# Performance work log

Hardware: AMD Instinct MI355X
Metric: run time of the kernel (lower is better)

## Reference

```python
import jax, jax.numpy as jnp
import numpy as np

N = 50000
E = 400000
NEG_SLOPE = 0.2


def gat_conv(x, src, dst, W, a_src, a_dst, b, heads, out_ch):
    """PyG-style GATConv with self-loops already included in (src, dst).
    src/dst: [E2] edge endpoints; messages flow src -> dst; softmax over in-edges per dst.
    """
    n = x.shape[0]
    h = (x @ W).reshape(n, heads, out_ch)               # [N, H, C]
    es = jnp.sum(h * a_src, axis=-1)                    # [N, H] alpha_src per node
    ed = jnp.sum(h * a_dst, axis=-1)                    # [N, H] alpha_dst per node
    e = jax.nn.leaky_relu(es[src] + ed[dst], NEG_SLOPE)  # [E2, H] raw scores
    # segment softmax over destination neighborhoods (stable)
    m = jax.ops.segment_max(e, dst, num_segments=n)     # [N, H]
    p = jnp.exp(e - m[dst])
    s = jax.ops.segment_sum(p, dst, num_segments=n)     # [N, H]
    alpha = p / s[dst]                                  # [E2, H]
    agg = jax.ops.segment_sum(h[src] * alpha[..., None], dst, num_segments=n)  # [N, H, C]
    return agg.reshape(n, heads * out_ch) + b


def setup_inputs() -> dict:
    key = jax.random.key(0)
    ks = jax.random.split(key, 14)
    rn = lambda k, shape, s=0.1: (jax.random.normal(k, shape, dtype=jnp.float32) * s)
    x = jax.random.normal(ks[0], (N, 21), dtype=jnp.float32)
    edge_index = jax.random.randint(ks[1], (2, E), 0, N, dtype=jnp.int32)
    return {
        "x": x,
        "W1": rn(ks[2], (21, 4 * 128)), "a_src1": rn(ks[3], (4, 128)), "a_dst1": rn(ks[4], (4, 128)), "b1": rn(ks[5], (512,)),
        "W2": rn(ks[6], (512, 64)), "a_src2": rn(ks[7], (1, 64)), "a_dst2": rn(ks[8], (1, 64)), "b2": rn(ks[9], (64,)),
        "W3": rn(ks[10], (64, 1)), "a_src3": rn(ks[11], (1, 1)), "a_dst3": rn(ks[12], (1, 1)), "b3": rn(ks[13], (1,)),
        "edge_index": edge_index,
    }


def reference(x, W1, a_src1, a_dst1, b1, W2, a_src2, a_dst2, b2, W3, a_src3, a_dst3, b3, edge_index):
    loops = jnp.arange(N, dtype=edge_index.dtype)
    src = jnp.concatenate([edge_index[0], loops])  # add self loops (PyG default)
    dst = jnp.concatenate([edge_index[1], loops])
    h1 = jax.nn.elu(gat_conv(x, src, dst, W1, a_src1, a_dst1, b1, heads=4, out_ch=128))   # [N, 512]
    h2 = jax.nn.elu(gat_conv(h1, src, dst, W2, a_src2, a_dst2, b2, heads=1, out_ch=64))   # [N, 64]
    h3 = gat_conv(h2, src, dst, W3, a_src3, a_dst3, b3, heads=1, out_ch=1)                # [N, 1]
    return h3.mean(axis=0)  # [1]
```

## Files before the change

### kernel.cpp

```cpp
#include <hip/hip_runtime.h>
#include <hip/hip_fp16.h>
#include <math.h>

#define N_NODES 50000
#define E_EDGES 400000
#define NEG_SLOPE 0.2f
#define SCAN_BLOCKS 250
#define SCAN_CHUNK 200

typedef _Float16 f16x8 __attribute__((ext_vector_type(8)));
typedef float f32x4 __attribute__((ext_vector_type(4)));

static inline int cdiv(long a, int b) { return (int)((a + b - 1) / b); }

__device__ __forceinline__ float lrelu(float v) {
    return v > 0.f ? v : NEG_SLOPE * v;
}

__device__ __forceinline__ void h4_to_f4(uint2 u, float o[4]) {
    union { uint2 u2; __half h[4]; } cv;
    cv.u2 = u;
    #pragma unroll
    for (int i = 0; i < 4; ++i) o[i] = __half2float(cv.h[i]);
}

__global__ void k_count(const int* __restrict__ ei, int* __restrict__ deg) {
    int e = blockIdx.x * blockDim.x + threadIdx.x;
    if (e >= E_EDGES) return;
    atomicAdd(&deg[ei[E_EDGES + e]], 1);
}

__global__ void k_scan1(const int* __restrict__ deg, int* __restrict__ bsum) {
    __shared__ int sd[256];
    int b = blockIdx.x, t = threadIdx.x;
    int lo = b * SCAN_CHUNK;
    int s = 0;
    for (int i = t; i < SCAN_CHUNK; i += 256) s += deg[lo + i];
    sd[t] = s;
    __syncthreads();
    for (int off = 128; off; off >>= 1) {
        if (t < off) sd[t] += sd[t + off];
        __syncthreads();
    }
    if (t == 0) bsum[b] = sd[0];
}

__global__ void k_scan2(int* __restrict__ bsum) {
    __shared__ int sd[256];
    int t = threadIdx.x;
    int v = (t < SCAN_BLOCKS) ? bsum[t] : 0;
    sd[t] = v;
    __syncthreads();
    for (int off = 1; off < 256; off <<= 1) {
        int u = (t >= off) ? sd[t - off] : 0;
        __syncthreads();
        sd[t] += u;
        __syncthreads();
    }
    if (t < SCAN_BLOCKS) bsum[t] = sd[t] - v;
}

__global__ void k_scan3(const int* __restrict__ deg, const int* __restrict__ bsum,
                        int* __restrict__ row_ptr) {
    __shared__ int sd[256];
    int b = blockIdx.x, t = threadIdx.x;
    int lo = b * SCAN_CHUNK;
    int v = (t < SCAN_CHUNK) ? deg[lo + t] : 0;
    sd[t] = v;
    __syncthreads();
    for (int off = 1; off < 256; off <<= 1) {
        int u = (t >= off) ? sd[t - off] : 0;
        __syncthreads();
        sd[t] += u;
        __syncthreads();
    }
    if (t < SCAN_CHUNK) row_ptr[lo + t] = bsum[b] + sd[t] - v;
    if (b == 0 && t == 0) row_ptr[N_NODES] = E_EDGES;
}

__global__ void k_scatter(const int* __restrict__ ei, const int* __restrict__ row_ptr,
                          int* __restrict__ pos, int* __restrict__ csr_src) {
    int e = blockIdx.x * blockDim.x + threadIdx.x;
    if (e >= E_EDGES) return;
    int src = ei[e], dst = ei[E_EDGES + e];
    int p = atomicAdd(&pos[dst], 1);
    csr_src[row_ptr[dst] + p] = src;
}

__global__ void k_l1_coef(const float* __restrict__ x, const float* __restrict__ W1,
                          const float* __restrict__ a_src, const float* __restrict__ a_dst,
                          float* __restrict__ es, float* __restrict__ ed) {
    __shared__ float wesS[88], wedS[88];
    const int t = threadIdx.x;
    if (t < 168) {
        int which = t / 84;
        int idx = t % 84;
        int k = idx >> 2, h = idx & 3;
        const float* a = which ? a_dst : a_src;
        float s = 0.f;
        for (int c = 0; c < 128; ++c)
            s += W1[k * 512 + h * 128 + c] * a[h * 128 + c];
        (which ? wedS : wesS)[idx] = s;
    }
    __syncthreads();

    int node = blockIdx.x * blockDim.x + t;
    if (node >= N_NODES) return;
    const float* xr = x + (size_t)node * 21;
    float e1[4] = {0.f, 0.f, 0.f, 0.f}, e2[4] = {0.f, 0.f, 0.f, 0.f};
    #pragma unroll
    for (int k = 0; k < 21; ++k) {
        float xv = xr[k];
        float4 a = *(const float4*)&wesS[k * 4];
        float4 b = *(const float4*)&wedS[k * 4];
        e1[0] += xv * a.x; e1[1] += xv * a.y; e1[2] += xv * a.z; e1[3] += xv * a.w;
        e2[0] += xv * b.x; e2[1] += xv * b.y; e2[2] += xv * b.z; e2[3] += xv * b.w;
    }
    *(float4*)&es[node * 4] = make_float4(e1[0], e1[1], e1[2], e1[3]);
    *(float4*)&ed[node * 4] = make_float4(e2[0], e2[1], e2[2], e2[3]);
}

__global__ void k_edge_l1x(const int* __restrict__ row_ptr, const int* __restrict__ csr_src,
                           const float* __restrict__ x, const float* __restrict__ es,
                           const float* __restrict__ ed, __half* __restrict__ y16) {
    int wid = (blockIdx.x * blockDim.x + threadIdx.x) >> 6;
    int l = threadIdx.x & 63;
    if (wid >= N_NODES) return;
    const int dst = wid;
    const int hh = l >> 4, sub = l & 15;
    const int beg = row_ptr[dst], end = row_ptr[dst + 1];
    const float eddg = ed[dst * 4 + hh];
    const float self_v = lrelu(es[dst * 4 + hh] + eddg);

    float s = 0.f;
    for (int k = beg + sub; k < end; k += 16)
        s += __expf(lrelu(es[csr_src[k] * 4 + hh] + eddg));
    #pragma unroll
    for (int off = 1; off < 16; off <<= 1) s += __shfl_xor(s, off, 64);
    float p_self = __expf(self_v);
    s += p_self;
    float inv_s = 1.f / s;

    float ih[4], eh[4], ph[4];
    #pragma unroll
    for (int h = 0; h < 4; ++h) {
        ih[h] = __shfl(inv_s, h * 16, 64);
        eh[h] = __shfl(eddg, h * 16, 64);
        ph[h] = __shfl(p_self, h * 16, 64);
    }

    const int g = l / 21;
    const int c = l - g * 21;
    const bool act = (l < 63);

    float xdv = (act && g == 0) ? x[(size_t)dst * 21 + c] : 0.f;
    float acc[4];
    #pragma unroll
    for (int h = 0; h < 4; ++h) acc[h] = ph[h] * ih[h] * xdv;

    if (act) {
        int k = beg + g;
        for (; k + 3 < end; k += 6) {
            int s0 = csr_src[k], s1 = csr_src[k + 3];
            float4 e0 = *(const float4*)&es[s0 * 4];
            float4 e1 = *(const float4*)&es[s1 * 4];
            float x0 = x[(size_t)s0 * 21 + c];
            float x1 = x[(size_t)s1 * 21 + c];
            #pragma unroll
            for (int h = 0; h < 4; ++h) {
                float a0 = __expf(lrelu((&e0.x)[h] + eh[h])) * ih[h];
                float a1 = __expf(lrelu((&e1.x)[h] + eh[h])) * ih[h];
                acc[h] += a0 * x0 + a1 * x1;
            }
        }
        if (k < end) {
            int s0 = csr_src[k];
            float4 e0 = *(const float4*)&es[s0 * 4];
            float x0 = x[(size_t)s0 * 21 + c];
            #pragma unroll
            for (int h = 0; h < 4; ++h) {
                float a0 = __expf(lrelu((&e0.x)[h] + eh[h])) * ih[h];
                acc[h] += a0 * x0;
            }
        }
    }

    #pragma unroll
    for (int h = 0; h < 4; ++h) {
        float a1 = __shfl(acc[h], (l + 21) & 63, 64);
        float a2 = __shfl(acc[h], (l + 42) & 63, 64);
        acc[h] += a1 + a2;
    }
    if (l < 32) {
        #pragma unroll
        for (int h = 0; h < 4; ++h) {
            float v = (l < 21) ? acc[h] : 0.f;
            y16[(size_t)dst * 128 + h * 32 + l] = __float2half_rn(v);
        }
    }
}

__global__ void k_wt(const float* __restrict__ W1, const float* __restrict__ W2,
                     __half* __restrict__ W1t, __half* __restrict__ W2t) {
    int idx = blockIdx.x * blockDim.x + threadIdx.x;
    if (idx < 512 * 32) {
        int n = idx >> 5, k = idx & 31;
        W1t[idx] = (k < 21) ? __float2half_rn(W1[k * 512 + n]) : __half(0.f);
    } else {
        int j = idx - 512 * 32;
        if (j < 512 * 64) {
            int k = j >> 6, n = j & 63;
            W2t[(size_t)n * 512 + k] = __float2half_rn(W2[j]);
        }
    }
}

__global__ void k_l12_fused(const __half* __restrict__ y16, const __half* __restrict__ W1t,
                            const float* __restrict__ b1, const __half* __restrict__ W2t,
                            const float* __restrict__ a_src, const float* __restrict__ a_dst,
                            __half* __restrict__ C16, float* __restrict__ es, float* __restrict__ ed) {
    __shared__ _Float16 As[32][520];
    __shared__ float p1s[32][4];
    __shared__ float p2s[32][4];

    const int t = threadIdx.x;
    const int l = t & 63;
    const int wv = t >> 6;
    const int row0 = blockIdx.x * 32;
    const int lr = l & 15;
    const int kg = l >> 4;

    const _Float16* Y = (const _Float16*)y16;
    const _Float16* B1 = (const _Float16*)W1t;

    int ra0 = row0 + lr;       ra0 = ra0 < N_NODES ? ra0 : N_NODES - 1;
    int ra1 = row0 + 16 + lr;  ra1 = ra1 < N_NODES ? ra1 : N_NODES - 1;

    f32x4 acc1[2][8];
    #pragma unroll
    for (int m = 0; m < 2; ++m)
        #pragma unroll
        for (int n = 0; n < 8; ++n) acc1[m][n] = (f32x4){0.f, 0.f, 0.f, 0.f};

    f16x8 a0 = *(const f16x8*)(Y + (size_t)ra0 * 128 + wv * 32 + kg * 8);
    f16x8 a1 = *(const f16x8*)(Y + (size_t)ra1 * 128 + wv * 32 + kg * 8);

    #pragma unroll
    for (int nt = 0; nt < 8; ++nt) {
        f16x8 bf = *(const f16x8*)(B1 + (size_t)(wv * 128 + nt * 16 + lr) * 32 + kg * 8);
        acc1[0][nt] = __builtin_amdgcn_mfma_f32_16x16x32_f16(a0, bf, acc1[0][nt], 0, 0, 0);
        acc1[1][nt] = __builtin_amdgcn_mfma_f32_16x16x32_f16(a1, bf, acc1[1][nt], 0, 0, 0);
    }

    float bb[8];
    #pragma unroll
    for (int nt = 0; nt < 8; ++nt) bb[nt] = b1[wv * 128 + nt * 16 + lr];

    #pragma unroll
    for (int m = 0; m < 2; ++m) {
        #pragma unroll
        for (int r = 0; r < 4; ++r) {
            int rl = m * 16 + kg * 4 + r;
            #pragma unroll
            for (int nt = 0; nt < 8; ++nt) {
                float v = acc1[m][nt][r] + bb[nt];
                v = v > 0.f ? v : __expf(v) - 1.f;
                As[rl][wv * 128 + nt * 16 + lr] = (_Float16)v;
            }
        }
    }
    __syncthreads();

    const _Float16* B2 = (const _Float16*)W2t;
    const int n_g = wv * 16 + lr;
    f32x4 acc2[2];
    acc2[0] = (f32x4){0.f, 0.f, 0.f, 0.f};
    acc2[1] = (f32x4){0.f, 0.f, 0.f, 0.f};

    for (int kb = 0; kb < 512; kb += 32) {
        f16x8 fa0 = *(const f16x8*)&As[lr][kb + kg * 8];
        f16x8 fa1 = *(const f16x8*)&As[16 + lr][kb + kg * 8];
        f16x8 bf = *(const f16x8*)(B2 + (size_t)n_g * 512 + kb + kg * 8);
        acc2[0] = __builtin_amdgcn_mfma_f32_16x16x32_f16(fa0, bf, acc2[0], 0, 0, 0);
        acc2[1] = __builtin_amdgcn_mfma_f32_16x16x32_f16(fa1, bf, acc2[1], 0, 0, 0);
    }

    const float asv = a_src[n_g];
    const float adv = a_dst[n_g];

    #pragma unroll
    for (int m = 0; m < 2; ++m) {
        #pragma unroll
        for (int r = 0; r < 4; ++r) {
            int rl = m * 16 + kg * 4 + r;
            int grow = row0 + rl;
            float cv = acc2[m][r];
            float p1 = cv * asv, p2 = cv * adv;
            #pragma unroll
            for (int off = 1; off < 16; off <<= 1) {
                p1 += __shfl_xor(p1, off, 64);
                p2 += __shfl_xor(p2, off, 64);
            }
            if (grow < N_NODES)
                C16[(size_t)grow * 64 + n_g] = __float2half_rn(cv);
            if (lr == 0) { p1s[rl][wv] = p1; p2s[rl][wv] = p2; }
        }
    }
    __syncthreads();

    if (t < 32) {
        int grow = row0 + t;
        if (grow < N_NODES) {
            es[grow] = p1s[t][0] + p1s[t][1] + p1s[t][2] + p1s[t][3];
            ed[grow] = p2s[t][0] + p2s[t][1] + p2s[t][2] + p2s[t][3];
        }
    }
}

__global__ void k_gat_edge_l2_l3(const int* __restrict__ row_ptr, const int* __restrict__ csr_src,
                                 const __half* __restrict__ h16, const float* __restrict__ es,
                                 const float* __restrict__ ed, const float* __restrict__ b,
                                 const float* __restrict__ W3, const float* __restrict__ a_src3,
                                 const float* __restrict__ a_dst3, float* __restrict__ h3,
                                 float* __restrict__ es3, float* __restrict__ ed3) {
    int wid = (blockIdx.x * blockDim.x + threadIdx.x) >> 6;
    int lane = threadIdx.x & 63;
    if (wid >= N_NODES) return;
    const int dst = wid;
    const int g = lane >> 4, sub = lane & 15;
    const int beg = row_ptr[dst], end = row_ptr[dst + 1];
    const float edd = ed[dst];
    const float self_v = lrelu(es[dst] + edd);

    float s = 0.f;
    for (int k = beg + lane; k < end; k += 64)
        s += __expf(lrelu(es[csr_src[k]] + edd));
    #pragma unroll
    for (int off = 32; off; off >>= 1) s += __shfl_xor(s, off, 64);
    float p_self = __expf(self_v);
    s += p_self;
    const float inv_s = 1.f / s;

    float acc[4] = {0.f, 0.f, 0.f, 0.f};
    if (g == 0) {
        uint2 r = *(const uint2*)(h16 + (size_t)dst * 64 + sub * 4);
        float hv[4]; h4_to_f4(r, hv);
        float a_self = p_self * inv_s;
        #pragma unroll
        for (int j = 0; j < 4; ++j) acc[j] = a_self * hv[j];
    }
    for (int k0 = beg; k0 < end; k0 += 4) {
        int k = k0 + g;
        if (k < end) {
            int src = csr_src[k];
            float alpha = __expf(lrelu(es[src] + edd)) * inv_s;
            uint2 r = *(const uint2*)(h16 + (size_t)src * 64 + sub * 4);
            float hv[4]; h4_to_f4(r, hv);
            #pragma unroll
            for (int j = 0; j < 4; ++j) acc[j] += alpha * hv[j];
        }
    }
    #pragma unroll
    for (int off = 16; off < 64; off <<= 1) {
        #pragma unroll
        for (int j = 0; j < 4; ++j) acc[j] += __shfl_xor(acc[j], off, 64);
    }

    float4 bv = *(const float4*)&b[sub * 4];
    float4 w3 = *(const float4*)&W3[sub * 4];
    float o0 = acc[0] + bv.x, o1 = acc[1] + bv.y, o2 = acc[2] + bv.z, o3 = acc[3] + bv.w;
    o0 = o0 > 0.f ? o0 : expm1f(o0);
    o1 = o1 > 0.f ? o1 : expm1f(o1);
    o2 = o2 > 0.f ? o2 : expm1f(o2);
    o3 = o3 > 0.f ? o3 : expm1f(o3);
    float pp = o0 * w3.x + o1 * w3.y + o2 * w3.z + o3 * w3.w;
    #pragma unroll
    for (int off = 1; off < 16; off <<= 1) pp += __shfl_xor(pp, off, 64);

    if (lane == 0) {
        h3[dst] = pp;
        es3[dst] = pp * a_src3[0];
        ed3[dst] = pp * a_dst3[0];
    }
}

__global__ void k_gat_edge_c1_mean(const int* __restrict__ row_ptr, const int* __restrict__ csr_src,
                                   const float* __restrict__ h, const float* __restrict__ es,
                                   const float* __restrict__ ed, const float* __restrict__ b3,
                                   float* __restrict__ out) {
    __shared__ float sdata[256];
    int dst = blockIdx.x * blockDim.x + threadIdx.x;
    float val = 0.f;
    if (dst < N_NODES) {
        int beg = row_ptr[dst], end = row_ptr[dst + 1];
        float edd = ed[dst];
        float self_v = lrelu(es[dst] + edd);
        float p = __expf(self_v);
        float s = p;
        float acc = p * h[dst];
        for (int k = beg; k < end; ++k) {
            int src = csr_src[k];
            float pv = __expf(lrelu(es[src] + edd));
            s += pv;
            acc += pv * h[src];
        }
        val = acc / s;
    }
    sdata[threadIdx.x] = val;
    __syncthreads();
    for (int sft = 128; sft > 0; sft >>= 1) {
        if (threadIdx.x < sft) sdata[threadIdx.x] += sdata[threadIdx.x + sft];
        __syncthreads();
    }
    if (threadIdx.x == 0) {
        float add = sdata[0] / (float)N_NODES;
        if (blockIdx.x == 0) add += b3[0];
        atomicAdd(out, add);
    }
}

extern "C" void kernel_launch(void* const* d_in, const int* in_sizes, int n_in,
                              void* d_out, int out_size, void* d_ws, size_t ws_size,
                              hipStream_t stream) {
    const float* x      = (const float*)d_in[0];
    const float* W1     = (const float*)d_in[1];
    const float* a_src1 = (const float*)d_in[2];
    const float* a_dst1 = (const float*)d_in[3];
    const float* b1     = (const float*)d_in[4];
    const float* W2     = (const float*)d_in[5];
    const float* a_src2 = (const float*)d_in[6];
    const float* a_dst2 = (const float*)d_in[7];
    const float* b2     = (const float*)d_in[8];
    const float* W3     = (const float*)d_in[9];
    const float* a_src3 = (const float*)d_in[10];
    const float* a_dst3 = (const float*)d_in[11];
    const float* b3     = (const float*)d_in[12];
    const int*   ei     = (const int*)d_in[13];
    float* out = (float*)d_out;

    const int BS = 256;
    const size_t N = N_NODES;

    float*  ws      = (float*)d_ws;
    __half* y16     = (__half*)ws;
    __half* h2_16   = (__half*)(ws + N * 64);
    float*  h3raw   = ws + N * 96;
    float*  es3     = h3raw + N;
    float*  ed3     = es3 + N;
    float*  es_buf  = ed3 + N;
    float*  ed_buf  = es_buf + N * 4;
    __half* W1t     = (__half*)(ed_buf + N * 4);
    __half* W2t     = (__half*)(ed_buf + N * 4 + 8192);
    int*    deg     = (int*)(ed_buf + N * 4 + 8192 + 16384);
    int*    row_ptr = deg + N;
    int*    csr_src = row_ptr + N + 1;
    int*    bsum    = csr_src + E_EDGES;

    hipMemsetAsync(deg, 0, N * sizeof(int), stream);
    k_count<<<cdiv(E_EDGES, BS), BS, 0, stream>>>(ei, deg);
    k_scan1<<<SCAN_BLOCKS, 256, 0, stream>>>(deg, bsum);
    k_scan2<<<1, 256, 0, stream>>>(bsum);
    k_scan3<<<SCAN_BLOCKS, 256, 0, stream>>>(deg, bsum, row_ptr);
    hipMemsetAsync(deg, 0, N * sizeof(int), stream);
    k_scatter<<<cdiv(E_EDGES, BS), BS, 0, stream>>>(ei, row_ptr, deg, csr_src);

    k_l1_coef<<<cdiv((long)N, BS), BS, 0, stream>>>(x, W1, a_src1, a_dst1, es_buf, ed_buf);
    k_edge_l1x<<<cdiv((long)N * 64, BS), BS, 0, stream>>>(row_ptr, csr_src, x, es_buf, ed_buf, y16);

    k_wt<<<cdiv(512 * 32 + 512 * 64, BS), BS, 0, stream>>>(W1, W2, W1t, W2t);
    k_l12_fused<<<cdiv(N_NODES, 32), 256, 0, stream>>>(y16, W1t, b1, W2t, a_src2, a_dst2, h2_16, es_buf, ed_buf);

    k_gat_edge_l2_l3<<<cdiv((long)N * 64, BS), BS, 0, stream>>>(row_ptr, csr_src, h2_16, es_buf, ed_buf,
                                                                b2, W3, a_src3, a_dst3, h3raw, es3, ed3);

    hipMemsetAsync(out, 0, sizeof(float), stream);
    k_gat_edge_c1_mean<<<cdiv((long)N, BS), BS, 0, stream>>>(row_ptr, csr_src, h3raw, es3, ed3, b3, out);
}
```

Before: 165.9 us.

## Fuse prep kernels, drop scatter memset, parallelize final layer edge loop

Merges degree counting, the weight transposes and the layer-1 coefficient computation into one prep kernel, removing two launches. The CSR scatter now increments row_ptr itself, so row_ptr ends up holding segment ends and consumers read begin from row_ptr[dst-1]; this drops the second memset and the separate position array. The final mean kernel now uses 16 lanes per destination with shuffle reductions instead of one thread per node. Trade-offs are a different CSR ordering within rows (already nondeterministic) and a __syncthreads inside a block-conditional branch in the prep kernel.

```diff
diff --git a/kernel.cpp b/kernel.cpp
--- a/kernel.cpp
+++ b/kernel.cpp
@@ -24,10 +24,56 @@
     for (int i = 0; i < 4; ++i) o[i] = __half2float(cv.h[i]);
 }
 
-__global__ void k_count(const int* __restrict__ ei, int* __restrict__ deg) {
-    int e = blockIdx.x * blockDim.x + threadIdx.x;
-    if (e >= E_EDGES) return;
-    atomicAdd(&deg[ei[E_EDGES + e]], 1);
+__global__ void k_prep(const int* __restrict__ ei, int* __restrict__ deg,
+                       const float* __restrict__ x, const float* __restrict__ W1,
+                       const float* __restrict__ a_src, const float* __restrict__ a_dst,
+                       float* __restrict__ es, float* __restrict__ ed,
+                       const float* __restrict__ W2, __half* __restrict__ W1t,
+                       __half* __restrict__ W2t) {
+    __shared__ float wesS[88], wedS[88];
+    const int t = threadIdx.x;
+    const int gid = blockIdx.x * blockDim.x + t;
+
+    if (gid < E_EDGES) atomicAdd(&deg[ei[E_EDGES + gid]], 1);
+
+    if (gid < 512 * 32) {
+        int n = gid >> 5, k = gid & 31;
+        W1t[gid] = (k < 21) ? __float2half_rn(W1[k * 512 + n]) : __half(0.f);
+    } else if (gid < 512 * 32 + 512 * 64) {
+        int j = gid - 512 * 32;
+        int k = j >> 6, n = j & 63;
+        W2t[(size_t)n * 512 + k] = __float2half_rn(W2[j]);
+    }
+
+    if (blockIdx.x < (N_NODES + 255) / 256) {
+        if (t < 168) {
+            int which = t / 84;
+            int idx = t % 84;
+            int k = idx >> 2, h = idx & 3;
+            const float* a = which ? a_dst : a_src;
+            float s = 0.f;
+            for (int c = 0; c < 128; ++c)
+                s += W1[k * 512 + h * 128 + c] * a[h * 128 + c];
+            (which ? wedS : wesS)[idx] = s;
+        }
+        __syncthreads();
+
+        int node = blockIdx.x * blockDim.x + t;
+        if (node < N_NODES) {
+            const float* xr = x + (size_t)node * 21;
+            float e1[4] = {0.f, 0.f, 0.f, 0.f}, e2[4] = {0.f, 0.f, 0.f, 0.f};
+            #pragma unroll
+            for (int k = 0; k < 21; ++k) {
+                float xv = xr[k];
+                float4 a = *(const float4*)&wesS[k * 4];
+                float4 b = *(const float4*)&wedS[k * 4];
+                e1[0] += xv * a.x; e1[1] += xv * a.y; e1[2] += xv * a.z; e1[3] += xv * a.w;
+                e2[0] += xv * b.x; e2[1] += xv * b.y; e2[2] += xv * b.z; e2[3] += xv * b.w;
+            }
+            *(float4*)&es[node * 4] = make_float4(e1[0], e1[1], e1[2], e1[3]);
+            *(float4*)&ed[node * 4] = make_float4(e2[0], e2[1], e2[2], e2[3]);
+        }
+    }
 }
 
 __global__ void k_scan1(const int* __restrict__ deg, int* __restrict__ bsum) {
@@ -75,49 +121,15 @@
         __syncthreads();
     }
     if (t < SCAN_CHUNK) row_ptr[lo + t] = bsum[b] + sd[t] - v;
-    if (b == 0 && t == 0) row_ptr[N_NODES] = E_EDGES;
-}
-
-__global__ void k_scatter(const int* __restrict__ ei, const int* __restrict__ row_ptr,
-                          int* __restrict__ pos, int* __restrict__ csr_src) {
+}
+
+__global__ void k_scatter(const int* __restrict__ ei, int* __restrict__ row_ptr,
+                          int* __restrict__ csr_src) {
     int e = blockIdx.x * blockDim.x + threadIdx.x;
     if (e >= E_EDGES) return;
     int src = ei[e], dst = ei[E_EDGES + e];
-    int p = atomicAdd(&pos[dst], 1);
-    csr_src[row_ptr[dst] + p] = src;
-}
-
-__global__ void k_l1_coef(const float* __restrict__ x, const float* __restrict__ W1,
-                          const float* __restrict__ a_src, const float* __restrict__ a_dst,
-                          float* __restrict__ es, float* __restrict__ ed) {
-    __shared__ float wesS[88], wedS[88];
-    const int t = threadIdx.x;
-    if (t < 168) {
-        int which = t / 84;
-        int idx = t % 84;
-        int k = idx >> 2, h = idx & 3;
-        const float* a = which ? a_dst : a_src;
-        float s = 0.f;
-        for (int c = 0; c < 128; ++c)
-            s += W1[k * 512 + h * 128 + c] * a[h * 128 + c];
-        (which ? wedS : wesS)[idx] = s;
-    }
-    __syncthreads();
-
-    int node = blockIdx.x * blockDim.x + t;
-    if (node >= N_NODES) return;
-    const float* xr = x + (size_t)node * 21;
-    float e1[4] = {0.f, 0.f, 0.f, 0.f}, e2[4] = {0.f, 0.f, 0.f, 0.f};
-    #pragma unroll
-    for (int k = 0; k < 21; ++k) {
-        float xv = xr[k];
-        float4 a = *(const float4*)&wesS[k * 4];
-        float4 b = *(const float4*)&wedS[k * 4];
-        e1[0] += xv * a.x; e1[1] += xv * a.y; e1[2] += xv * a.z; e1[3] += xv * a.w;
-        e2[0] += xv * b.x; e2[1] += xv * b.y; e2[2] += xv * b.z; e2[3] += xv * b.w;
-    }
-    *(float4*)&es[node * 4] = make_float4(e1[0], e1[1], e1[2], e1[3]);
-    *(float4*)&ed[node * 4] = make_float4(e2[0], e2[1], e2[2], e2[3]);
+    int p = atomicAdd(&row_ptr[dst], 1);
+    csr_src[p] = src;
 }
 
 __global__ void k_edge_l1x(const int* __restrict__ row_ptr, const int* __restrict__ csr_src,
@@ -128,7 +140,8 @@
     if (wid >= N_NODES) return;
     const int dst = wid;
     const int hh = l >> 4, sub = l & 15;
-    const int beg = row_ptr[dst], end = row_ptr[dst + 1];
+    const int beg = dst ? row_ptr[dst - 1] : 0;
+    const int end = row_ptr[dst];
     const float eddg = ed[dst * 4 + hh];
     const float self_v = lrelu(es[dst * 4 + hh] + eddg);
 
@@ -196,21 +209,6 @@
         for (int h = 0; h < 4; ++h) {
             float v = (l < 21) ? acc[h] : 0.f;
             y16[(size_t)dst * 128 + h * 32 + l] = __float2half_rn(v);
-        }
-    }
-}
-
-__global__ void k_wt(const float* __restrict__ W1, const float* __restrict__ W2,
-                     __half* __restrict__ W1t, __half* __restrict__ W2t) {
-    int idx = blockIdx.x * blockDim.x + threadIdx.x;
-    if (idx < 512 * 32) {
-        int n = idx >> 5, k = idx & 31;
-        W1t[idx] = (k < 21) ? __float2half_rn(W1[k * 512 + n]) : __half(0.f);
-    } else {
-        int j = idx - 512 * 32;
-        if (j < 512 * 64) {
-            int k = j >> 6, n = j & 63;
-            W2t[(size_t)n * 512 + k] = __float2half_rn(W2[j]);
         }
     }
 }
@@ -328,7 +326,8 @@
     if (wid >= N_NODES) return;
     const int dst = wid;
     const int g = lane >> 4, sub = lane & 15;
-    const int beg = row_ptr[dst], end = row_ptr[dst + 1];
+    const int beg = dst ? row_ptr[dst - 1] : 0;
+    const int end = row_ptr[dst];
     const float edd = ed[dst];
     const float self_v = lrelu(es[dst] + edd);
 
@@ -389,30 +388,41 @@
                                    const float* __restrict__ ed, const float* __restrict__ b3,
                                    float* __restrict__ out) {
     __shared__ float sdata[256];
-    int dst = blockIdx.x * blockDim.x + threadIdx.x;
+    const int t = threadIdx.x;
+    const int gid = blockIdx.x * 256 + t;
+    const int dst = gid >> 4;
+    const int sub = t & 15;
     float val = 0.f;
     if (dst < N_NODES) {
-        int beg = row_ptr[dst], end = row_ptr[dst + 1];
+        int beg = dst ? row_ptr[dst - 1] : 0;
+        int end = row_ptr[dst];
         float edd = ed[dst];
-        float self_v = lrelu(es[dst] + edd);
-        float p = __expf(self_v);
-        float s = p;
-        float acc = p * h[dst];
-        for (int k = beg; k < end; ++k) {
+        float s = 0.f, acc = 0.f;
+        for (int k = beg + sub; k < end; k += 16) {
             int src = csr_src[k];
             float pv = __expf(lrelu(es[src] + edd));
             s += pv;
             acc += pv * h[src];
         }
-        val = acc / s;
-    }
-    sdata[threadIdx.x] = val;
+        #pragma unroll
+        for (int off = 1; off < 16; off <<= 1) {
+            s += __shfl_xor(s, off, 64);
+            acc += __shfl_xor(acc, off, 64);
+        }
+        if (sub == 0) {
+            float p = __expf(lrelu(es[dst] + edd));
+            s += p;
+            acc += p * h[dst];
+            val = acc / s;
+        }
+    }
+    sdata[t] = val;
     __syncthreads();
     for (int sft = 128; sft > 0; sft >>= 1) {
-        if (threadIdx.x < sft) sdata[threadIdx.x] += sdata[threadIdx.x + sft];
-        __syncthreads();
-    }
-    if (threadIdx.x == 0) {
+        if (t < sft) sdata[t] += sdata[t + sft];
+        __syncthreads();
+    }
+    if (t == 0) {
         float add = sdata[0] / (float)N_NODES;
         if (blockIdx.x == 0) add += b3[0];
         atomicAdd(out, add);
@@ -453,26 +463,25 @@
     __half* W2t     = (__half*)(ed_buf + N * 4 + 8192);
     int*    deg     = (int*)(ed_buf + N * 4 + 8192 + 16384);
     int*    row_ptr = deg + N;
-    int*    csr_src = row_ptr + N + 1;
+    int*    csr_src = row_ptr + N;
     int*    bsum    = csr_src + E_EDGES;
 
     hipMemsetAsync(deg, 0, N * sizeof(int), stream);
-    k_count<<<cdiv(E_EDGES, BS), BS, 0, stream>>>(ei, deg);
+    k_prep<<<cdiv(E_EDGES, BS), BS, 0, stream>>>(ei, deg, x, W1, a_src1, a_dst1,
+                                                 es_buf, ed_buf, W2, W1t, W2t);
+
     k_scan1<<<SCAN_BLOCKS, 256, 0, stream>>>(deg, bsum);
     k_scan2<<<1, 256, 0, stream>>>(bsum);
     k_scan3<<<SCAN_BLOCKS, 256, 0, stream>>>(deg, bsum, row_ptr);
-    hipMemsetAsync(deg, 0, N * sizeof(int), stream);
-    k_scatter<<<cdiv(E_EDGES, BS), BS, 0, stream>>>(ei, row_ptr, deg, csr_src);
-
-    k_l1_coef<<<cdiv((long)N, BS), BS, 0, stream>>>(x, W1, a_src1, a_dst1, es_buf, ed_buf);
+    k_scatter<<<cdiv(E_EDGES, BS), BS, 0, stream>>>(ei, row_ptr, csr_src);
+
     k_edge_l1x<<<cdiv((long)N * 64, BS), BS, 0, stream>>>(row_ptr, csr_src, x, es_buf, ed_buf, y16);
 
-    k_wt<<<cdiv(512 * 32 + 512 * 64, BS), BS, 0, stream>>>(W1, W2, W1t, W2t);
     k_l12_fused<<<cdiv(N_NODES, 32), 256, 0, stream>>>(y16, W1t, b1, W2t, a_src2, a_dst2, h2_16, es_buf, ed_buf);
 
     k_gat_edge_l2_l3<<<cdiv((long)N * 64, BS), BS, 0, stream>>>(row_ptr, csr_src, h2_16, es_buf, ed_buf,
                                                                 b2, W3, a_src3, a_dst3, h3raw, es3, ed3);
 
     hipMemsetAsync(out, 0, sizeof(float), stream);
-    k_gat_edge_c1_mean<<<cdiv((long)N, BS), BS, 0, stream>>>(row_ptr, csr_src, h3raw, es3, ed3, b3, out);
-}
+    k_gat_edge_c1_mean<<<cdiv((long)N * 16, BS), BS, 0, stream>>>(row_ptr, csr_src, h3raw, es3, ed3, b3, out);
+}
```

After: 194.0 us. +16.9%, slower.
